# Optimization experiments

Hardware: AMD Instinct MI355X
Metric: run time of the kernel (lower is better)

The kernel has to match this reference:

```python
import jax, jax.numpy as jnp
import numpy as np

IMAGE_SIZE = 256
DET = int(IMAGE_SIZE * 2 ** 0.5 + 0.5)  # 362 detector bins (diagonal coverage)
US = 4
N_ACQ = 45                     # acquired views: 0,4,...,176 degrees
N_FULL = (N_ACQ - 1) * US + 1  # 177 full (upsampled) views


def setup_inputs() -> dict:
    key = jax.random.key(0)
    k1, k2 = jax.random.split(key)
    x_source = jax.random.normal(k1, (2, 1, IMAGE_SIZE, IMAGE_SIZE), jnp.float32)
    s_target = jax.random.normal(k2, (2, 1, DET, N_ACQ), jnp.float32)
    theta_acq = np.arange(0, 180, 4, dtype=np.float64)  # 45 acquired angles
    segs = [np.linspace(theta_acq[i], theta_acq[i + 1], US + 1)[:-1] for i in range(N_ACQ - 1)]
    theta_full = np.concatenate(segs + [theta_acq[-1:]]).astype(np.float32)  # [177]
    acq_idx = (np.arange(N_ACQ) * US).astype(np.int32)  # positions of acquired angles in theta_full
    return {"x_source": x_source, "s_target": s_target,
            "thetas_deg": jnp.asarray(theta_full), "acq_idx": jnp.asarray(acq_idx)}


def bilinear_gather(img, xs, ys):
    # img: [B,C,H,W]; xs, ys: pixel coords [A,det,det]; zero outside the image.
    H, W = img.shape[-2], img.shape[-1]
    x0 = jnp.floor(xs); y0 = jnp.floor(ys)
    wx = xs - x0; wy = ys - y0
    x0i = x0.astype(jnp.int32); y0i = y0.astype(jnp.int32)

    def get(yi, xi):
        valid = (xi >= 0) & (xi < W) & (yi >= 0) & (yi < H)
        v = img[:, :, jnp.clip(yi, 0, H - 1), jnp.clip(xi, 0, W - 1)]  # [B,C,A,det,det]
        return jnp.where(valid, v, 0.0)

    return (get(y0i, x0i) * (1 - wy) * (1 - wx)
            + get(y0i, x0i + 1) * (1 - wy) * wx
            + get(y0i + 1, x0i) * wy * (1 - wx)
            + get(y0i + 1, x0i + 1) * wy * wx)


def radon(x, thetas_rad, det):
    # Ray-sum projection: sino[theta, t] = sum_s image(t*cos - s*sin, t*sin + s*cos)
    B, C, H, W = x.shape
    t = jnp.arange(det, dtype=x.dtype) - (det - 1) / 2.0  # centered detector/ray coord
    cos = jnp.cos(thetas_rad)[:, None, None]
    sin = jnp.sin(thetas_rad)[:, None, None]
    T = t[None, :, None]; S = t[None, None, :]
    xs = T * cos - S * sin + (W - 1) / 2.0  # [A,det,det]
    ys = T * sin + S * cos + (H - 1) / 2.0
    return bilinear_gather(x, xs, ys).sum(-1)  # [B,C,A,det]


def ramp_filter(size):
    # skimage/pytorch_radon style ramp built from its real-space kernel
    n = np.concatenate([np.arange(1, size // 2 + 1, 2), np.arange(size // 2 - 1, 0, -2)])
    f = np.zeros(size)
    f[0] = 0.25
    f[1::2] = -1.0 / (np.pi * n) ** 2
    return jnp.asarray(2 * np.real(np.fft.fft(f)), dtype=jnp.float32)


def fbp(sino, thetas_rad, image_size):
    # Filtered back-projection. sino: [B,C,det,A]
    B, C, det, A = sino.shape
    pad = max(64, int(2 ** np.ceil(np.log2(2 * det))))
    filt = ramp_filter(pad)  # [pad]
    sp = jnp.pad(sino, ((0, 0), (0, 0), (0, pad - det), (0, 0)))
    sf = jnp.fft.ifft(jnp.fft.fft(sp, axis=2) * filt[None, None, :, None], axis=2).real
    sf = jnp.transpose(sf[:, :, :det, :], (0, 1, 3, 2)).astype(sino.dtype)  # [B,C,A,det]
    g = jnp.arange(image_size, dtype=sino.dtype) - (image_size - 1) / 2.0
    cos = jnp.cos(thetas_rad); sin = jnp.sin(thetas_rad)
    # detector coordinate hit by each pixel, per angle: t = x*cos + y*sin
    t = (cos[:, None, None] * g[None, None, :]
         + sin[:, None, None] * g[None, :, None] + (det - 1) / 2.0)  # [A,H,W]
    t = t.reshape(A, -1)
    t0 = jnp.floor(t)
    w = t - t0
    t0i = t0.astype(jnp.int32)
    aidx = jnp.arange(A)[:, None]

    def samp(ti):
        valid = (ti >= 0) & (ti < det)
        return jnp.where(valid, sf[:, :, aidx, jnp.clip(ti, 0, det - 1)], 0.0)  # [B,C,A,HW]

    v = samp(t0i) * (1 - w) + samp(t0i + 1) * w
    reco = v.sum(2) * (jnp.pi / (2 * A))
    return reco.reshape(B, C, image_size, image_size)


def reference(x_source, s_target, thetas_deg, acq_idx):
    th = thetas_deg * (jnp.pi / 180.0)
    s = radon(x_source, th, DET)          # [B,C,A,det]
    s = jnp.transpose(s, (0, 1, 3, 2))    # [B,C,det,A] -- angle axis last, as in the module
    # masked data-consistency update: acquired columns become (target - predicted)
    s = s.at[..., acq_idx].set(s_target - s[..., acq_idx])
    return fbp(s, th, IMAGE_SIZE)
```

## Files before the change

### kernel.cpp

```cpp
#include <hip/hip_runtime.h>
#include <math.h>

#define IMG   256
#define NFULL 177
#define DETN  362
#define NACQ  45
#define PAD   1024

#define SINO_OFF 0
#define SF_OFF   131072

#define HALF_T 180.5f
#define SEGL   16
#define TILE_W 640

__constant__ const int kStripOrd4[48] =
    {22,23,21,24, 20,25,19,26, 18,27,17,28, 16,29,15,30,
     14,31,13,32, 12,33,11,34, 10,35, 9,36,  8,37, 7,38,
      6,39, 5,40,  4,41, 3,42,  2,43, 1,44,  0,45,-1,-1};

__device__ __forceinline__ void gload16(const float* g, float* l) {
    __builtin_amdgcn_global_load_lds(
        (const __attribute__((address_space(1))) void*)g,
        (__attribute__((address_space(3))) void*)l, 16, 0, 0);
}

template<int P>
__device__ __forceinline__ float2 radon_strip2(
    const float* __restrict__ img0,
    const float* __restrict__ img1,
    float* tb,
    const float c, const float s,
    const float xbase, const float ybase,
    const float xAB_mn, const float yAB_mn, const float yAB_mx,
    const int Slo, const int Shi, const int lane)
{
    constexpr int W4   = P / 4;
    constexpr int HMAX = TILE_W / P;
    const int ts = lane & 7;
    float val0 = 0.0f, val1 = 0.0f;

    for (int Sseg = Slo; Sseg < Shi; Sseg += SEGL) {
        const float sv0 = (float)Sseg - HALF_T;
        const float sv1 = sv0 + (float)(SEGL - 1);
        const float xmn = xAB_mn - sv1 * s;
        const float ya  = sv0 * c, yb = sv1 * c;
        const float ymn = yAB_mn + fminf(ya, yb);
        const float ymx = yAB_mx + fmaxf(ya, yb);
        const int ix0  = (int)floorf(xmn) - 1;
        const int iy0  = (int)floorf(ymn) - 1;
        const int ix0a = ix0 & ~3;
        const int h    = min((int)floorf(ymx) + 3 - iy0, HMAX);
        const int total4 = W4 * h;
        const int nfull  = total4 & ~63;
        const bool interior = (ix0a >= 0) & (iy0 >= 0) &
                              (ix0a + P <= IMG) & (iy0 + h <= IMG);

        asm volatile("s_waitcnt lgkmcnt(0)" ::: "memory");

        if (interior) {
            const int base0 = iy0 * IMG + ix0a;
            for (int f0 = 0; f0 < nfull; f0 += 64) {
                const int f  = f0 + lane;
                const int r  = f / W4;
                const int c4 = f - r * W4;
                const int go = base0 + r * IMG + (c4 << 2);
                gload16(img0 + go, tb + (f0 << 2));
                gload16(img1 + go, tb + TILE_W + (f0 << 2));
            }
            const int f = nfull + lane;
            if (f < total4) {
                const int r  = f / W4;
                const int c4 = f - r * W4;
                const int go = base0 + r * IMG + (c4 << 2);
                gload16(img0 + go, tb + (nfull << 2));
                gload16(img1 + go, tb + TILE_W + (nfull << 2));
            }
        } else {
            for (int f = lane; f < total4; f += 64) {
                const int r  = f / W4;
                const int c4 = f - r * W4;
                const int gy = iy0 + r;
                const int gx = ix0a + (c4 << 2);
                const bool ok = ((unsigned)gy < (unsigned)IMG) &
                                ((unsigned)gx <= (unsigned)(IMG - 4));
                float4 v0 = make_float4(0.f, 0.f, 0.f, 0.f);
                float4 v1 = v0;
                if (ok) {
                    const int go = gy * IMG + gx;
                    v0 = *(const float4*)(img0 + go);
                    v1 = *(const float4*)(img1 + go);
                }
                *(float4*)(tb + (f << 2)) = v0;
                *(float4*)(tb + TILE_W + (f << 2)) = v1;
            }
        }
        asm volatile("s_waitcnt vmcnt(0) lgkmcnt(0)" ::: "memory");
        __builtin_amdgcn_sched_barrier(0);

        const float xoff = xbase - (float)ix0a;
        const float yoff = ybase - (float)iy0;
        const int Send = min(Sseg + SEGL, Shi);

        auto samp = [&](float sval) {
            const float xs  = fmaf(-sval, s, xoff);
            const float ys  = fmaf(sval, c, yoff);
            const float x0f = floorf(xs);
            const float y0f = floorf(ys);
            const float wx  = xs - x0f;
            const float wy  = ys - y0f;
            const int base = (int)fmaf(y0f, (float)P, x0f);
            const float a00 = tb[base];
            const float a01 = tb[base + 1];
            const float a10 = tb[base + P];
            const float a11 = tb[base + P + 1];
            const float b00 = tb[TILE_W + base];
            const float b01 = tb[TILE_W + base + 1];
            const float b10 = tb[TILE_W + base + P];
            const float b11 = tb[TILE_W + base + P + 1];
            const float ah0 = fmaf(wx, a01 - a00, a00);
            const float ah1 = fmaf(wx, a11 - a10, a10);
            val0 += fmaf(wy, ah1 - ah0, ah0);
            const float bh0 = fmaf(wx, b01 - b00, b00);
            const float bh1 = fmaf(wx, b11 - b10, b10);
            val1 += fmaf(wy, bh1 - bh0, bh0);
        };

        if (Send - Sseg == SEGL) {
            const float s0 = (float)(Sseg + ts) - HALF_T;
            #pragma unroll
            for (int u = 0; u < SEGL / 8; ++u) samp(s0 + (float)(8 * u));
        } else {
            for (int S = Sseg + ts; S < Send; S += 8) samp((float)S - HALF_T);
        }
    }
    return make_float2(val0, val1);
}

__global__ __launch_bounds__(256, 8) void radon_kernel(
    const float* __restrict__ x,
    const float* __restrict__ thetas,
    float* __restrict__ sino)
{
    const int a = blockIdx.x;
    const int w    = threadIdx.x >> 6;
    const int lane = threadIdx.x & 63;
    const int sp   = kStripOrd4[blockIdx.y * 4 + w];
    if (sp < 0) return;
    const int T0   = sp << 3;
    const int tt   = lane >> 3;
    const int ts   = lane & 7;
    const int T    = T0 + tt;

    __shared__ __align__(16) float tile[4][2 * TILE_W];
    float* tb = tile[w];

    const float th = thetas[a] * (float)(M_PI / 180.0);
    const float c = cosf(th);
    const float s = sinf(th);
    const float cx = (IMG - 1) * 0.5f;
    const float cy = (IMG - 1) * 0.5f;
    const float Tc = (float)T - HALF_T;
    const float xbase = Tc * c + cx;
    const float ybase = Tc * s + cy;

    float lo = -1e30f, hi = 1e30f;
    bool empty = (T >= DETN);
    {   const float aa = -s;
        if (aa > 1e-5f)       { lo = fmaxf(lo, (-1.0f - xbase) / aa); hi = fminf(hi, (256.0f - xbase) / aa); }
        else if (aa < -1e-5f) { lo = fmaxf(lo, (256.0f - xbase) / aa); hi = fminf(hi, (-1.0f - xbase) / aa); }
        else if (xbase <= -1.0f || xbase >= 256.0f) empty = true;
    }
    {   const float aa = c;
        if (aa > 1e-5f)       { lo = fmaxf(lo, (-1.0f - ybase) / aa); hi = fminf(hi, (256.0f - ybase) / aa); }
        else if (aa < -1e-5f) { lo = fmaxf(lo, (256.0f - ybase) / aa); hi = fminf(hi, (-1.0f - ybase) / aa); }
        else if (ybase <= -1.0f || ybase >= 256.0f) empty = true;
    }
    lo = fmaxf(lo, -200.0f);
    hi = fminf(hi, 200.0f);
    int Slo = max(0, (int)floorf(lo + HALF_T) - 1);
    int Shi = min(DETN, (int)floorf(hi + HALF_T) + 2);
    if (empty || Shi < Slo) { Slo = 0; Shi = 0; }

    int wlo = (Shi > Slo) ? Slo : DETN;
    int whi = (Shi > Slo) ? Shi : 0;
    #pragma unroll
    for (int d = 1; d < 64; d <<= 1) {
        wlo = min(wlo, __shfl_xor(wlo, d, 64));
        whi = max(whi, __shfl_xor(whi, d, 64));
    }

    int best = 2;
    {
        const float ac = fabsf(c), as = fabsf(s);
        const float spanx = 7.f * ac + 15.f * as;
        const float spany = 7.f * as + 15.f * ac;
        const float Pc[4] = {20.f, 24.f, 28.f, 32.f};
        const int   Hm[4] = {32, 26, 22, 20};
        int bcost = 1 << 30;
        #pragma unroll
        for (int p = 0; p < 4; ++p) {
            const float Pf = Pc[p];
            const float dT = s * Pf + c;
            const float dS = c * Pf - s;
            const int bank = (int)floorf((float)tt * dT + (float)ts * dS + 0.5f) & 31;
            unsigned long long m = ~0ull;
            #pragma unroll
            for (int bit = 0; bit < 5; ++bit) {
                const unsigned long long bb = __ballot((bank >> bit) & 1);
                m &= ((bank >> bit) & 1) ? bb : ~bb;
            }
            int cnt = __popcll(m);
            #pragma unroll
            for (int d = 1; d < 64; d <<= 1) cnt = max(cnt, __shfl_xor(cnt, d, 64));
            const bool fit = (spanx <= Pf - 8.05f) && (spany <= (float)Hm[p] - 5.05f);
            if (fit && cnt < bcost) { bcost = cnt; best = p; }
        }
    }

    const float TcA = (float)T0 - HALF_T;
    const float TcB = (float)(T0 + 7) - HALF_T;
    const float xAB_mn = fminf(TcA * c + cx, TcB * c + cx);
    const float yAB_mn = fminf(TcA * s + cy, TcB * s + cy);
    const float yAB_mx = fmaxf(TcA * s + cy, TcB * s + cy);

    const float* __restrict__ img0 = x;
    const float* __restrict__ img1 = x + IMG * IMG;

    float2 val;
    switch (best) {
    case 0:  val = radon_strip2<20>(img0, img1, tb, c, s, xbase, ybase,
                                    xAB_mn, yAB_mn, yAB_mx, wlo, whi, lane); break;
    case 1:  val = radon_strip2<24>(img0, img1, tb, c, s, xbase, ybase,
                                    xAB_mn, yAB_mn, yAB_mx, wlo, whi, lane); break;
    case 2:  val = radon_strip2<28>(img0, img1, tb, c, s, xbase, ybase,
                                    xAB_mn, yAB_mn, yAB_mx, wlo, whi, lane); break;
    default: val = radon_strip2<32>(img0, img1, tb, c, s, xbase, ybase,
                                    xAB_mn, yAB_mn, yAB_mx, wlo, whi, lane); break;
    }

    val.x += __shfl_xor(val.x, 1, 8);
    val.x += __shfl_xor(val.x, 2, 8);
    val.x += __shfl_xor(val.x, 4, 8);
    val.y += __shfl_xor(val.y, 1, 8);
    val.y += __shfl_xor(val.y, 2, 8);
    val.y += __shfl_xor(val.y, 4, 8);
    if (ts == 0 && T < DETN) {
        sino[a * DETN + T] = val.x;
        sino[(NFULL + a) * DETN + T] = val.y;
    }
}

__global__ __launch_bounds__(192) void dc_filter_kernel(
    const float* __restrict__ sino,
    const float* __restrict__ st,
    const int*   __restrict__ acq,
    float* __restrict__ sf)
{
    const int blk = blockIdx.x;
    const int b = blk / NFULL;
    const int a = blk - b * NFULL;
    const int tid = threadIdx.x;

    __shared__ float col[DETN];
    __shared__ float gf[PAD];

    const float SC = (float)(M_PI / (2.0 * NFULL));
    const float c0 = 0.5f * SC;
    for (int n = tid; n < PAD; n += 192) {
        float v = 0.0f;
        if (n & 1) {
            const int d = (n < PAD - n) ? n : (PAD - n);
            const float pd = (float)M_PI * (float)d;
            v = -2.0f / (pd * pd) * SC;
        }
        gf[n] = v;
    }

    int inv = -1;
    for (int i = 0; i < NACQ; ++i) {
        if (acq[i] == a) inv = i;
    }

    for (int m = tid; m < DETN; m += 192) {
        float val = sino[(b * NFULL + a) * DETN + m];
        if (inv >= 0) {
            val = st[(b * DETN + m) * NACQ + inv] - val;
        }
        col[m] = val;
    }
    __syncthreads();

    const int T = blockIdx.y * 181 + tid;
    if (tid < 181) {
        const int m0 = (T + 1) & 1;
        float acc = c0 * col[T];
        #pragma unroll 4
        for (int k = 0; k < 181; ++k) {
            const int m = m0 + 2 * k;
            acc += col[m] * gf[(T - m) & (PAD - 1)];
        }
        sf[(b * NFULL + a) * DETN + T] = acc;
    }
}

__global__ __launch_bounds__(256) void backproject_kernel(
    const float* __restrict__ sf,
    const float* __restrict__ thetas,
    float* __restrict__ out)
{
    __shared__ float cb[2 * NFULL];
    __shared__ float red[256];
    const int tid = threadIdx.x;
    const int lane  = tid & 63;
    const int phase = tid >> 6;
    const int pix = blockIdx.x * 64 + lane;
    const int b = pix >> 16;
    const int y = (pix >> 8) & 255;
    const int xq = pix & 255;
    const float gx = (float)xq - (IMG - 1) * 0.5f;
    const float gy = (float)y  - (IMG - 1) * 0.5f;

    for (int a = tid; a < NFULL; a += 256) {
        float th = thetas[a] * (float)(M_PI / 180.0);
        cb[2 * a]     = cosf(th);
        cb[2 * a + 1] = fmaf(sinf(th), gy, HALF_T);
    }
    __syncthreads();

    const float* __restrict__ sfb = sf + b * NFULL * DETN;

    float acc = 0.0f;
    #pragma unroll 4
    for (int a = phase; a < NFULL; a += 4) {
        const float cs = cb[2 * a];
        const float bs = cb[2 * a + 1];
        const float t = fmaf(cs, gx, bs);
        const float t0f = floorf(t);
        const float w = t - t0f;
        const float* row = sfb + a * DETN + (int)t0f;
        const float v0 = row[0];
        const float v1 = row[1];
        acc += v0 + w * (v1 - v0);
    }
    red[tid] = acc;
    __syncthreads();
    if (tid < 64) {
        out[blockIdx.x * 64 + tid] =
            red[tid] + red[tid + 64] + red[tid + 128] + red[tid + 192];
    }
}

extern "C" void kernel_launch(void* const* d_in, const int* in_sizes, int n_in,
                              void* d_out, int out_size, void* d_ws, size_t ws_size,
                              hipStream_t stream) {
    const float* x      = (const float*)d_in[0];
    const float* st     = (const float*)d_in[1];
    const float* thetas = (const float*)d_in[2];
    const int*   acq    = (const int*)d_in[3];
    float* out  = (float*)d_out;
    float* wsf  = (float*)d_ws;
    float* sino = wsf + SINO_OFF;
    float* sf   = wsf + SF_OFF;

    dim3 gA(NFULL, 12);
    radon_kernel<<<gA, 256, 0, stream>>>(x, thetas, sino);
    dim3 gB(2 * NFULL, 2);
    dc_filter_kernel<<<gB, 192, 0, stream>>>(sino, st, acq, sf);
    backproject_kernel<<<(2 * IMG * IMG) / 64, 256, 0, stream>>>(sf, thetas, out);
}
```

Before: 115.6 us.

## Split each radon ray strip across four waves along the integration axis

Each block now handles one 8-ray strip, and the four waves each integrate a quarter of the ray segments instead of each wave owning its own strip. Partial sums are combined through shared memory after a barrier. This raises the block count from 12 to 46 per angle and shortens each wave's serial loop, aiming at better latency hiding and load balance. In exchange it adds a __syncthreads and a shared-memory reduction, and the tile buffer is reused for the partial sums.

```diff
diff --git a/kernel.cpp b/kernel.cpp
--- a/kernel.cpp
+++ b/kernel.cpp
@@ -14,10 +14,9 @@
 #define SEGL   16
 #define TILE_W 640
 
-__constant__ const int kStripOrd4[48] =
-    {22,23,21,24, 20,25,19,26, 18,27,17,28, 16,29,15,30,
-     14,31,13,32, 12,33,11,34, 10,35, 9,36,  8,37, 7,38,
-      6,39, 5,40,  4,41, 3,42,  2,43, 1,44,  0,45,-1,-1};
+__constant__ const int kStripOrd[46] =
+    {22,23,21,24,20,25,19,26,18,27,17,28,16,29,15,30,14,31,13,32,
+     12,33,11,34,10,35,9,36,8,37,7,38,6,39,5,40,4,41,3,42,2,43,1,44,0,45};
 
 __device__ __forceinline__ void gload16(const float* g, float* l) {
     __builtin_amdgcn_global_load_lds(
@@ -145,8 +144,7 @@
     const int a = blockIdx.x;
     const int w    = threadIdx.x >> 6;
     const int lane = threadIdx.x & 63;
-    const int sp   = kStripOrd4[blockIdx.y * 4 + w];
-    if (sp < 0) return;
+    const int sp   = kStripOrd[blockIdx.y];
     const int T0   = sp << 3;
     const int tt   = lane >> 3;
     const int ts   = lane & 7;
@@ -189,6 +187,12 @@
         wlo = min(wlo, __shfl_xor(wlo, d, 64));
         whi = max(whi, __shfl_xor(whi, d, 64));
     }
+
+    const int range = max(whi - wlo, 0);
+    const int nseg  = (range + SEGL - 1) / SEGL;
+    const int per   = (nseg + 3) >> 2;
+    const int q_lo  = wlo + w * per * SEGL;
+    const int q_hi  = min(q_lo + per * SEGL, whi);
 
     int best = 2;
     {
@@ -230,13 +234,13 @@
     float2 val;
     switch (best) {
     case 0:  val = radon_strip2<20>(img0, img1, tb, c, s, xbase, ybase,
-                                    xAB_mn, yAB_mn, yAB_mx, wlo, whi, lane); break;
+                                    xAB_mn, yAB_mn, yAB_mx, q_lo, q_hi, lane); break;
     case 1:  val = radon_strip2<24>(img0, img1, tb, c, s, xbase, ybase,
-                                    xAB_mn, yAB_mn, yAB_mx, wlo, whi, lane); break;
+                                    xAB_mn, yAB_mn, yAB_mx, q_lo, q_hi, lane); break;
     case 2:  val = radon_strip2<28>(img0, img1, tb, c, s, xbase, ybase,
-                                    xAB_mn, yAB_mn, yAB_mx, wlo, whi, lane); break;
+                                    xAB_mn, yAB_mn, yAB_mx, q_lo, q_hi, lane); break;
     default: val = radon_strip2<32>(img0, img1, tb, c, s, xbase, ybase,
-                                    xAB_mn, yAB_mn, yAB_mx, wlo, whi, lane); break;
+                                    xAB_mn, yAB_mn, yAB_mx, q_lo, q_hi, lane); break;
     }
 
     val.x += __shfl_xor(val.x, 1, 8);
@@ -245,9 +249,20 @@
     val.y += __shfl_xor(val.y, 1, 8);
     val.y += __shfl_xor(val.y, 2, 8);
     val.y += __shfl_xor(val.y, 4, 8);
-    if (ts == 0 && T < DETN) {
-        sino[a * DETN + T] = val.x;
-        sino[(NFULL + a) * DETN + T] = val.y;
+
+    if (ts == 0) {
+        tb[2 * tt]     = val.x;
+        tb[2 * tt + 1] = val.y;
+    }
+    __syncthreads();
+    if (w == 0 && lane < 16) {
+        const float sum = tile[0][lane] + tile[1][lane]
+                        + tile[2][lane] + tile[3][lane];
+        const int T2 = T0 + (lane >> 1);
+        const int bb = lane & 1;
+        if (T2 < DETN) {
+            sino[(bb * NFULL + a) * DETN + T2] = sum;
+        }
     }
 }
 
@@ -363,7 +378,7 @@
     float* sino = wsf + SINO_OFF;
     float* sf   = wsf + SF_OFF;
 
-    dim3 gA(NFULL, 12);
+    dim3 gA(NFULL, 46);
     radon_kernel<<<gA, 256, 0, stream>>>(x, thetas, sino);
     dim3 gB(2 * NFULL, 2);
     dc_filter_kernel<<<gB, 192, 0, stream>>>(sino, st, acq, sf);
```

Measured after the change: 122.7 us. 6.1% more time.
